# Kernel optimization log

Measured on AMD Instinct MI355X. Metric: run time of the kernel, lower is better.

## Reference

```python
import jax, jax.numpy as jnp
import numpy as np
import math

B, N, IN_DIM, HID, OUT = 16, 1024, 3, 32, 4
RATIO = 0.2
K1 = math.ceil(RATIO * N)    # 205 nodes kept after pool 1
K2 = math.ceil(RATIO * K1)   # 41 nodes kept after pool 2
AVG_DEG = 16.0
BN_EPS = 1e-5


def setup_inputs() -> dict:
    key = jax.random.key(0)
    ks = jax.random.split(key, 16)
    x = jax.random.normal(ks[0], (B, N, IN_DIM), jnp.float32)
    # sparse random undirected adjacency (binary edge weights = 1), no self loops
    u = jax.random.uniform(ks[1], (B, N, N))
    A = (u < (AVG_DEG / N)).astype(jnp.float32)
    A = jnp.maximum(A, jnp.swapaxes(A, -1, -2))
    A = A * (1.0 - jnp.eye(N, dtype=jnp.float32))
    g = lambda i, shp: (jax.random.normal(ks[i], shp, jnp.float32) * 0.1)
    params = dict(
        Wd0=g(2, (IN_DIM, HID)), bd0=jnp.zeros((HID,), jnp.float32),
        Wd1=g(3, (HID, HID)),    bd1=jnp.zeros((HID,), jnp.float32),
        Wd2=g(4, (HID, HID)),    bd2=jnp.zeros((HID,), jnp.float32),
        Wu0=g(5, (HID, HID)),    bu0=jnp.zeros((HID,), jnp.float32),
        Wu1=g(6, (HID, HID)),    bu1=jnp.zeros((HID,), jnp.float32),
        p1=g(7, (HID,)), p2=g(8, (HID,)),
        gamma=jnp.ones((HID,), jnp.float32), beta=jnp.zeros((HID,), jnp.float32),
        W1=g(9, (HID, HID)),  b1=jnp.zeros((HID,), jnp.float32),
        W2=g(10, (HID, HID)), b2=jnp.zeros((HID,), jnp.float32),
        W3=g(11, (HID, OUT)), b3=jnp.zeros((OUT,), jnp.float32),
    )
    return {"x": x, "adj": A, **params}


def _gcn(A, x, W, b):
    # GCNConv(improved=True): A_hat = A + 2I, symmetric normalization
    n = A.shape[-1]
    A_hat = A + 2.0 * jnp.eye(n, dtype=A.dtype)
    deg = A_hat.sum(-1)                              # [B, n]
    dis = jnp.where(deg > 0, jax.lax.rsqrt(deg), 0.0)
    A_norm = dis[..., :, None] * A_hat * dis[..., None, :]
    return jnp.einsum('bij,bjf->bif', A_norm, x @ W) + b


def _augment(A):
    # GraphUNet.augment_adj: add self loops (w=1), square adjacency, drop diag
    n = A.shape[-1]
    eye = jnp.eye(n, dtype=A.dtype)
    Bm = A + eye
    A2 = jnp.einsum('bij,bjk->bik', Bm, Bm)
    return A2 * (1.0 - eye)


def _topk_pool(A, x, p, k):
    # TopKPooling: score = tanh(x.p / ||p||), keep top-k nodes per graph
    score = jnp.tanh((x @ p) / jnp.linalg.norm(p))   # [B, n]
    vals, perm = jax.lax.top_k(score, k)             # descending, matches PyG
    bidx = jnp.arange(x.shape[0])[:, None]
    x_p = x[bidx, perm] * vals[..., None]
    A_p = A[bidx[..., None], perm[:, :, None], perm[:, None, :]]
    return A_p, x_p, perm


def reference(x, adj, Wd0, bd0, Wd1, bd1, Wd2, bd2, Wu0, bu0, Wu1, bu1,
              p1, p2, gamma, beta, W1, b1, W2, b2, W3, b3):
    bidx = jnp.arange(x.shape[0])[:, None]
    # ---- GraphUNet down path ----
    h0 = jax.nn.relu(_gcn(adj, x, Wd0, bd0))
    A1, h, perm1 = _topk_pool(_augment(adj), h0, p1, K1)
    h1 = jax.nn.relu(_gcn(A1, h, Wd1, bd1))
    A2, h, perm2 = _topk_pool(_augment(A1), h1, p2, K2)
    h = jax.nn.relu(_gcn(A2, h, Wd2, bd2))
    # ---- up path (sum_res=True) ----
    up = jnp.zeros_like(h1).at[bidx, perm2].set(h)
    h = jax.nn.relu(_gcn(A1, h1 + up, Wu0, bu0))
    up = jnp.zeros_like(h0).at[bidx, perm1].set(h)
    h = _gcn(adj, h0 + up, Wu1, bu1)   # last up conv: no activation
    # ---- BatchNorm1d over all nodes (training-mode batch stats, biased var) ----
    mean = h.mean((0, 1))
    var = h.var((0, 1))
    hn = (h - mean) * jax.lax.rsqrt(var + BN_EPS) * gamma + beta
    # ---- outnetwork MLP (dropout = identity in eval), LeakyReLU slope 0.01 ----
    r = jax.nn.leaky_relu(hn @ W1 + b1)
    r = jax.nn.leaky_relu(r @ W2 + b2)
    r = r @ W3 + b3
    return r.at[..., 0].set(jax.nn.sigmoid(r[..., 0]))
```

## Files before the change

kernel.cpp:

```cpp
#include <hip/hip_runtime.h>
#include <cmath>

#define BB 16
#define NN 1024
#define KK1 205
#define KK2 42
#define CAP 96
#define CHUNKS1 52
#define NREP 64

__global__ void k_deg_csr(const float* __restrict__ adj, const float* __restrict__ x,
                          const float* __restrict__ W,
                          float* __restrict__ dis0, int* __restrict__ ncnt,
                          int* __restrict__ nbr, unsigned long long* __restrict__ mask,
                          float* __restrict__ dxw, float* __restrict__ pacc) {
  if (blockIdx.x == 0) {
    for (int q = threadIdx.x; q < NREP * 64; q += 256) pacc[q] = 0.f;
  }
  int row = blockIdx.x * 4 + (threadIdx.x >> 6);
  int lane = threadIdx.x & 63;
  const float* ar = adj + (size_t)row * NN;
  float v[16];
#pragma unroll
  for (int c = 0; c < 16; ++c) v[c] = ar[c * 64 + lane];
  int base = 0;
  int* nr = nbr + (size_t)row * CAP;
#pragma unroll
  for (int c = 0; c < 16; ++c) {
    unsigned long long m = __ballot(v[c] != 0.0f);
    if (lane == c) mask[(size_t)row * 16 + c] = m;
    if (v[c] != 0.0f) {
      int pos = base + __popcll(m & ((1ull << lane) - 1ull));
      if (pos < CAP) nr[pos] = c * 64 + lane;
    }
    base += __popcll(m);
  }
  float dis = rsqrtf((float)base + 2.0f);
  if (lane == 0) {
    ncnt[row] = base < CAP ? base : CAP;
    dis0[row] = dis;
  }
  if (lane < 32) {
    float x0 = x[row * 3], x1 = x[row * 3 + 1], x2 = x[row * 3 + 2];
    float s = x0 * W[lane] + x1 * W[32 + lane] + x2 * W[64 + lane];
    dxw[(size_t)row * 32 + lane] = s * dis;
  }
}

template<bool RELU, bool SCORE, bool BNSTATS>
__global__ __launch_bounds__(256) void k_spmm_lds(
    const float* __restrict__ dxw, const float* __restrict__ dis,
    const int* __restrict__ ncnt, const int* __restrict__ nbr,
    const float* __restrict__ bias, float* __restrict__ out,
    float* __restrict__ score, const float* __restrict__ p,
    float* __restrict__ pacc) {
  __shared__ float sdxw[NN * 32];
  __shared__ float bs[8][32], bq[8][32];
  int tid = threadIdx.x;
  int b = blockIdx.x >> 4, chunk = blockIdx.x & 15;
  {
    const float4* src = (const float4*)(dxw + ((size_t)b * NN) * 32);
    float4* dst = (float4*)sdxw;
    for (int q = tid; q < NN * 8; q += 256) dst[q] = src[q];
  }
  __syncthreads();
  int g = tid >> 5, f = tid & 31;
  float bia = bias[f];
  float pv = SCORE ? p[f] : 0.f;
  float S = 0.f, Q = 0.f;
#pragma unroll
  for (int it = 0; it < 8; ++it) {
    int li = chunk * 64 + g * 8 + it;
    int node = b * NN + li;
    int cnt = ncnt[node];
    const int* lst = nbr + (size_t)node * CAP;
    float a0 = 0.f, a1 = 0.f, a2 = 0.f, a3 = 0.f;
    int k = 0;
    for (; k + 4 <= cnt; k += 4) {
      int4 j4 = *(const int4*)(lst + k);
      a0 += sdxw[j4.x * 32 + f];
      a1 += sdxw[j4.y * 32 + f];
      a2 += sdxw[j4.z * 32 + f];
      a3 += sdxw[j4.w * 32 + f];
    }
    for (; k < cnt; ++k) a0 += sdxw[lst[k] * 32 + f];
    float acc = (a0 + a1) + (a2 + a3) + 2.0f * sdxw[li * 32 + f];
    float r = dis[node] * acc + bia;
    if (RELU) r = fmaxf(r, 0.f);
    out[(size_t)node * 32 + f] = r;
    if (SCORE) {
      float d = r * pv, pp = pv * pv;
#pragma unroll
      for (int o = 16; o; o >>= 1) { d += __shfl_xor(d, o, 32); pp += __shfl_xor(pp, o, 32); }
      if (f == 0) score[node] = tanhf(d / sqrtf(pp));
    }
    if (BNSTATS) { S += r; Q += r * r; }
  }
  if (BNSTATS) {
    bs[g][f] = S; bq[g][f] = Q;
    __syncthreads();
    if (tid < 32) {
      float SS = 0.f, QQ = 0.f;
#pragma unroll
      for (int q = 0; q < 8; ++q) { SS += bs[q][tid]; QQ += bq[q][tid]; }
      int rep = blockIdx.x & (NREP - 1);
      atomicAdd(&pacc[rep * 64 + tid], SS);
      atomicAdd(&pacc[rep * 64 + 32 + tid], QQ);
    }
  }
}

__global__ __launch_bounds__(256) void k_sortA1(
    const unsigned long long* __restrict__ mask, const float* __restrict__ score1,
    const float* __restrict__ h0, const float* __restrict__ Wd1,
    float* __restrict__ A1, float* __restrict__ dis1, float* __restrict__ t1,
    int* __restrict__ inv1) {
  __shared__ union {
    unsigned long long skey[1024];
    unsigned long long smT[16 * KK1];
  } sm;
  __shared__ int sp[KK1];
  __shared__ float sval[KK1];
  int blk = blockIdx.x;
  int b = blk / CHUNKS1, chunk = blk - b * CHUNKS1;
  int t = threadIdx.x;
  for (int idx = t; idx < 1024; idx += 256) {
    float v = score1[b * NN + idx];
    unsigned int u = __float_as_uint(v);
    if (u == 0x80000000u) u = 0u;
    unsigned int ordv = (u & 0x80000000u) ? ~u : (u | 0x80000000u);
    if (chunk == 0) inv1[b * NN + idx] = -1;
    sm.skey[idx] = ((unsigned long long)(~ordv) << 32) | (unsigned)idx;
  }
  __syncthreads();
  for (int k = 2; k <= 1024; k <<= 1)
    for (int j = k >> 1; j > 0; j >>= 1) {
      for (int idx = t; idx < 1024; idx += 256) {
        int ixj = idx ^ j;
        if (ixj > idx) {
          unsigned long long a = sm.skey[idx], c = sm.skey[ixj];
          bool up = ((idx & k) == 0);
          if (up == (a > c)) { sm.skey[idx] = c; sm.skey[ixj] = a; }
        }
      }
      __syncthreads();
    }
  if (t < KK1) {
    unsigned long long kk = sm.skey[t];
    unsigned int ord = ~(unsigned int)(kk >> 32);
    unsigned int u = (ord & 0x80000000u) ? (ord & 0x7FFFFFFFu) : ~ord;
    int src = (int)(kk & 0xFFFFFFFFull);
    sp[t] = src;
    sval[t] = __uint_as_float(u);
    if (chunk == 0) inv1[b * NN + src] = t;
  }
  __syncthreads();
  for (int q = t; q < KK1 * 16; q += 256) {
    int i = q >> 4, w = q & 15;
    sm.smT[w * KK1 + i] = mask[((size_t)(b * NN + sp[i])) * 16 + w];
  }
  __syncthreads();
  int wave = t >> 6, lane = t & 63;
  int i = chunk * 4 + wave;
  if (i < KK1) {
    unsigned long long r[16];
#pragma unroll
    for (int w = 0; w < 16; ++w) r[w] = sm.smT[w * KK1 + i];
    float rowsum = 0.f;
    for (int j = lane; j < KK1; j += 64) {
      int cnt = 0;
#pragma unroll
      for (int w = 0; w < 16; ++w) cnt += __popcll(r[w] & sm.smT[w * KK1 + j]);
      int pj = sp[j];
      float edge = (float)((r[pj >> 6] >> (pj & 63)) & 1ull);
      float v = (j == i) ? 0.f : ((float)cnt + 2.f * edge);
      A1[((size_t)(b * KK1) + i) * KK1 + j] = v;
      rowsum += v;
    }
#pragma unroll
    for (int o = 32; o; o >>= 1) rowsum += __shfl_xor(rowsum, o);
    float dis = rsqrtf(rowsum + 2.0f);
    if (lane == 0) dis1[b * KK1 + i] = dis;
    if (lane < 32) {
      const float* hr = h0 + (size_t)(b * NN + sp[i]) * 32;
      float s = 0.f;
#pragma unroll
      for (int k = 0; k < 32; ++k) s += hr[k] * Wd1[k * 32 + lane];
      t1[((size_t)(b * KK1) + i) * 32 + lane] = s * dis * sval[i];
    }
  }
}

template<bool RELU, bool SCORE>
__global__ __launch_bounds__(256) void k_dense_apply(
    const float* __restrict__ A, const float* __restrict__ tbuf,
    const float* __restrict__ dis, const float* __restrict__ bias,
    int M, float* __restrict__ out, float* __restrict__ score,
    const float* __restrict__ p) {
  int row = blockIdx.x;
  int b = row / M, i = row - b * M;
  int tid = threadIdx.x;
  int g = tid >> 5, f = tid & 31;
  const float* Ar = A + (size_t)row * M;
  const float* tb = tbuf + (size_t)b * M * 32;
  float acc = 0.f;
  for (int j = g; j < M; j += 8)
    acc += Ar[j] * tb[j * 32 + f];
  __shared__ float ls[8][32];
  ls[g][f] = acc;
  __syncthreads();
  if (tid < 32) {
    float s = 0.f;
#pragma unroll
    for (int q = 0; q < 8; ++q) s += ls[q][tid];
    s += 2.0f * tb[i * 32 + tid];
    float r = dis[row] * s + bias[tid];
    if (RELU) r = fmaxf(r, 0.f);
    out[(size_t)row * 32 + tid] = r;
    if (SCORE) {
      float pv = p[tid];
      float d = r * pv, pp = pv * pv;
#pragma unroll
      for (int o = 16; o; o >>= 1) { d += __shfl_xor(d, o, 32); pp += __shfl_xor(pp, o, 32); }
      if (tid == 0) score[row] = tanhf(d / sqrtf(pp));
    }
  }
}

__global__ __launch_bounds__(256) void k_buildA2s(
    const float* __restrict__ score2, const float* __restrict__ A1,
    const float* __restrict__ h1, const float* __restrict__ Wd2,
    float* __restrict__ A2, float* __restrict__ dis2, float* __restrict__ t2,
    int* __restrict__ inv2) {
  __shared__ unsigned long long skey[256];
  __shared__ int sp2[KK2];
  __shared__ float sv2[KK2];
  __shared__ float gsum[8];
  __shared__ float ds2s;
  int row = blockIdx.x;
  int b = row / KK2, i = row - b * KK2;
  int t = threadIdx.x;
  {
    unsigned int ordv;
    if (t < KK1) {
      float v = score2[b * KK1 + t];
      unsigned int u = __float_as_uint(v);
      if (u == 0x80000000u) u = 0u;
      ordv = (u & 0x80000000u) ? ~u : (u | 0x80000000u);
      if (i == 0) inv2[b * KK1 + t] = -1;
    } else ordv = 0u;
    skey[t] = ((unsigned long long)(~ordv) << 32) | (unsigned)t;
  }
  __syncthreads();
  for (int k = 2; k <= 256; k <<= 1)
    for (int j = k >> 1; j > 0; j >>= 1) {
      int ixj = t ^ j;
      if (ixj > t) {
        unsigned long long a = skey[t], c = skey[ixj];
        bool up = ((t & k) == 0);
        if (up == (a > c)) { skey[t] = c; skey[ixj] = a; }
      }
      __syncthreads();
    }
  if (t < KK2) {
    unsigned long long kk = skey[t];
    unsigned int ord = ~(unsigned int)(kk >> 32);
    unsigned int u = (ord & 0x80000000u) ? (ord & 0x7FFFFFFFu) : ~ord;
    int src = (int)(kk & 0xFFFFFFFFull);
    sp2[t] = src;
    sv2[t] = __uint_as_float(u);
    if (i == 0) inv2[b * KK1 + src] = t;
  }
  __syncthreads();
  int g = t >> 5, lane = t & 31;
  int pi = sp2[i];
  const float* Ri = A1 + ((size_t)(b * KK1 + pi)) * KK1;
  float part = 0.f;
  for (int j = g; j < KK2; j += 8) {
    const float* Rj = A1 + ((size_t)(b * KK1 + sp2[j])) * KK1;
    float s = 0.f;
    for (int k = lane; k < KK1; k += 32) s += Ri[k] * Rj[k];
#pragma unroll
    for (int o = 16; o; o >>= 1) s += __shfl_xor(s, o, 32);
    float v = (i == j) ? 0.f : (s + 2.0f * Ri[sp2[j]]);
    if (lane == 0) {
      A2[(size_t)row * KK2 + j] = v;
      part += v;
    }
  }
  if (lane == 0) gsum[g] = part;
  __syncthreads();
  if (t == 0) {
    float s = 0.f;
#pragma unroll
    for (int q = 0; q < 8; ++q) s += gsum[q];
    float d2 = rsqrtf(s + 2.0f);
    dis2[row] = d2;
    ds2s = d2;
  }
  __syncthreads();
  if (t < 32) {
    const float* hr = h1 + (size_t)(b * KK1 + pi) * 32;
    float s = 0.f;
#pragma unroll
    for (int k = 0; k < 32; ++k) s += hr[k] * Wd2[k * 32 + t];
    t2[(size_t)row * 32 + t] = s * ds2s * sv2[i];
  }
}

__global__ void k_xw32u(const float* __restrict__ h, const float* __restrict__ up,
                        const int* __restrict__ inv, const float* __restrict__ W,
                        const float* __restrict__ dis, int M, int K,
                        float* __restrict__ out) {
  int idx = blockIdx.x * 256 + threadIdx.x;
  int f = idx & 31; int node = idx >> 5;
  int b = node / M;
  int iv = inv[node];
  const float* xr = h + (size_t)node * 32;
  float s = 0.f;
  if (iv >= 0) {
    const float* ur = up + (size_t)(b * K + iv) * 32;
#pragma unroll
    for (int k = 0; k < 32; ++k) s += (xr[k] + ur[k]) * W[k * 32 + f];
  } else {
#pragma unroll
    for (int k = 0; k < 32; ++k) s += xr[k] * W[k * 32 + f];
  }
  out[idx] = s * dis[node];
}

__global__ __launch_bounds__(64) void k_mlp(
    const float* __restrict__ h, const float* __restrict__ pacc,
    const float* __restrict__ gamma, const float* __restrict__ beta,
    const float* __restrict__ W1, const float* __restrict__ b1,
    const float* __restrict__ W2, const float* __restrict__ b2,
    const float* __restrict__ W3, const float* __restrict__ b3,
    float* __restrict__ out) {
  __shared__ float sW1[1024], sW2[1024], sW3[128];
  __shared__ float sb1[32], sb2[32], sb3[4], sscale[32], sshift[32];
  __shared__ float red[64];
  int t = threadIdx.x;
  {
    const float4* W1v = (const float4*)W1; float4* d1 = (float4*)sW1;
#pragma unroll
    for (int i = 0; i < 4; ++i) d1[t + i * 64] = W1v[t + i * 64];
    const float4* W2v = (const float4*)W2; float4* d2 = (float4*)sW2;
#pragma unroll
    for (int i = 0; i < 4; ++i) d2[t + i * 64] = W2v[t + i * 64];
    if (t < 32) ((float4*)sW3)[t] = ((const float4*)W3)[t];
    if (t < 32) { sb1[t] = b1[t]; sb2[t] = b2[t]; }
    if (t < 4) sb3[t] = b3[t];
    float a0 = 0.f, a1 = 0.f, a2 = 0.f, a3 = 0.f;
#pragma unroll
    for (int rep = 0; rep < NREP; rep += 4) {
      a0 += pacc[(rep + 0) * 64 + t]; a1 += pacc[(rep + 1) * 64 + t];
      a2 += pacc[(rep + 2) * 64 + t]; a3 += pacc[(rep + 3) * 64 + t];
    }
    red[t] = (a0 + a1) + (a2 + a3);
  }
  __syncthreads();
  if (t < 32) {
    const float inv = 1.0f / (float)(BB * NN);
    float m = red[t] * inv;
    float v = red[32 + t] * inv - m * m;
    float sc = gamma[t] * rsqrtf(v + 1e-5f);
    sscale[t] = sc;
    sshift[t] = beta[t] - m * sc;
  }
  __syncthreads();
  int node = blockIdx.x * 64 + t;
  const float4* hr = (const float4*)(h + (size_t)node * 32);
  float hn[32];
#pragma unroll
  for (int i = 0; i < 8; ++i) {
    float4 x = hr[i];
    hn[i * 4 + 0] = x.x * sscale[i * 4 + 0] + sshift[i * 4 + 0];
    hn[i * 4 + 1] = x.y * sscale[i * 4 + 1] + sshift[i * 4 + 1];
    hn[i * 4 + 2] = x.z * sscale[i * 4 + 2] + sshift[i * 4 + 2];
    hn[i * 4 + 3] = x.w * sscale[i * 4 + 3] + sshift[i * 4 + 3];
  }
  float r1[32];
#pragma unroll
  for (int f = 0; f < 32; ++f) r1[f] = sb1[f];
#pragma unroll
  for (int k = 0; k < 32; ++k) {
    float a = hn[k];
#pragma unroll
    for (int f = 0; f < 32; ++f) r1[f] += a * sW1[k * 32 + f];
  }
#pragma unroll
  for (int f = 0; f < 32; ++f) r1[f] = r1[f] > 0.f ? r1[f] : 0.01f * r1[f];
  float r2[32];
#pragma unroll
  for (int f = 0; f < 32; ++f) r2[f] = sb2[f];
#pragma unroll
  for (int k = 0; k < 32; ++k) {
    float a = r1[k];
#pragma unroll
    for (int f = 0; f < 32; ++f) r2[f] += a * sW2[k * 32 + f];
  }
#pragma unroll
  for (int f = 0; f < 32; ++f) r2[f] = r2[f] > 0.f ? r2[f] : 0.01f * r2[f];
  float r3[4];
#pragma unroll
  for (int c = 0; c < 4; ++c) r3[c] = sb3[c];
#pragma unroll
  for (int k = 0; k < 32; ++k) {
    float a = r2[k];
#pragma unroll
    for (int c = 0; c < 4; ++c) r3[c] += a * sW3[k * 4 + c];
  }
  float4 o;
  o.x = 1.0f / (1.0f + expf(-r3[0]));
  o.y = r3[1]; o.z = r3[2]; o.w = r3[3];
  ((float4*)out)[node] = o;
}

extern "C" void kernel_launch(void* const* d_in, const int* in_sizes, int n_in,
                              void* d_out, int out_size, void* d_ws, size_t ws_size,
                              hipStream_t stream) {
  const float* x    = (const float*)d_in[0];
  const float* adj  = (const float*)d_in[1];
  const float* Wd0  = (const float*)d_in[2];
  const float* bd0  = (const float*)d_in[3];
  const float* Wd1  = (const float*)d_in[4];
  const float* bd1  = (const float*)d_in[5];
  const float* Wd2  = (const float*)d_in[6];
  const float* bd2  = (const float*)d_in[7];
  const float* Wu0  = (const float*)d_in[8];
  const float* bu0  = (const float*)d_in[9];
  const float* Wu1  = (const float*)d_in[10];
  const float* bu1  = (const float*)d_in[11];
  const float* p1   = (const float*)d_in[12];
  const float* p2   = (const float*)d_in[13];
  const float* gamma= (const float*)d_in[14];
  const float* beta = (const float*)d_in[15];
  const float* W1   = (const float*)d_in[16];
  const float* b1   = (const float*)d_in[17];
  const float* W2   = (const float*)d_in[18];
  const float* b2   = (const float*)d_in[19];
  const float* W3   = (const float*)d_in[20];
  const float* b3   = (const float*)d_in[21];
  float* out = (float*)d_out;

  char* w = (char*)d_ws;
  auto alloc = [&](size_t bytes) -> void* {
    void* p = (void*)w;
    w += (bytes + 255) & ~(size_t)255;
    return p;
  };
  float* dis0 = (float*)alloc(BB * NN * 4);
  int*   ncnt = (int*)alloc(BB * NN * 4);
  int*   nbr  = (int*)alloc((size_t)BB * NN * CAP * 4);
  unsigned long long* mask = (unsigned long long*)alloc((size_t)BB * NN * 16 * 8);
  float* dxw  = (float*)alloc((size_t)BB * NN * 32 * 4);
  float* h0   = (float*)alloc((size_t)BB * NN * 32 * 4);
  float* score1 = (float*)alloc(BB * NN * 4);
  int*   inv1 = (int*)alloc(BB * NN * 4);
  float* A1   = (float*)alloc((size_t)BB * KK1 * KK1 * 4);
  float* dis1 = (float*)alloc(BB * KK1 * 4);
  float* t1   = (float*)alloc((size_t)BB * KK1 * 32 * 4);
  float* h1   = (float*)alloc((size_t)BB * KK1 * 32 * 4);
  float* score2 = (float*)alloc(BB * KK1 * 4);
  int*   inv2 = (int*)alloc(BB * KK1 * 4);
  float* A2   = (float*)alloc((size_t)BB * KK2 * KK2 * 4);
  float* dis2 = (float*)alloc(BB * KK2 * 4);
  float* t2   = (float*)alloc((size_t)BB * KK2 * 32 * 4);
  float* h2   = (float*)alloc((size_t)BB * KK2 * 32 * 4);
  float* hu0  = (float*)alloc((size_t)BB * KK1 * 32 * 4);
  float* hfin = (float*)alloc((size_t)BB * NN * 32 * 4);
  float* pacc = (float*)alloc((size_t)NREP * 64 * 4);

  const int TOT_N32  = BB * NN * 32;
  const int TOT_K132 = BB * KK1 * 32;

  k_deg_csr<<<BB * NN / 4, 256, 0, stream>>>(adj, x, Wd0, dis0, ncnt, nbr, mask, dxw, pacc);
  k_spmm_lds<true, true, false><<<BB * 16, 256, 0, stream>>>(
      dxw, dis0, ncnt, nbr, bd0, h0, score1, p1, nullptr);
  k_sortA1<<<BB * CHUNKS1, 256, 0, stream>>>(mask, score1, h0, Wd1, A1, dis1, t1, inv1);
  k_dense_apply<true, true><<<BB * KK1, 256, 0, stream>>>(
      A1, t1, dis1, bd1, KK1, h1, score2, p2);
  k_buildA2s<<<BB * KK2, 256, 0, stream>>>(score2, A1, h1, Wd2, A2, dis2, t2, inv2);
  k_dense_apply<true, false><<<BB * KK2, 256, 0, stream>>>(
      A2, t2, dis2, bd2, KK2, h2, nullptr, nullptr);
  k_xw32u<<<TOT_K132 / 256, 256, 0, stream>>>(h1, h2, inv2, Wu0, dis1, KK1, KK2, t1);
  k_dense_apply<true, false><<<BB * KK1, 256, 0, stream>>>(
      A1, t1, dis1, bu0, KK1, hu0, nullptr, nullptr);
  k_xw32u<<<TOT_N32 / 256, 256, 0, stream>>>(h0, hu0, inv1, Wu1, dis0, NN, KK1, dxw);
  k_spmm_lds<false, false, true><<<BB * 16, 256, 0, stream>>>(
      dxw, dis0, ncnt, nbr, bu1, hfin, nullptr, nullptr, pacc);
  k_mlp<<<BB * NN / 64, 64, 0, stream>>>(hfin, pacc, gamma, beta,
                                         W1, b1, W2, b2, W3, b3, out);
}
```

Baseline: 343.1 us.

## Fuse final up-path transform into SpMM and use register/shuffle bitonic sorts

The separate k_xw32u launch for the last up-path layer is removed. k_spmm_fused now loads h0, hu0 and inv1 into LDS and computes (h0+up)·Wu1·dis in place before the sparse aggregation and batch-norm statistics. Each of the 16 chunk blocks per graph recomputes the full 1024-row transform, trading redundant arithmetic for one fewer launch and one fewer global round trip. The top-k bitonic sorts in k_sortA1 and k_buildA2s keep keys in registers and exchange them with wave shuffles, touching LDS only for strides of 64 or more, which cuts barrier count. LDS use in the fused kernel sits near the per-workgroup limit.

```diff
diff --git a/kernel.cpp b/kernel.cpp
--- a/kernel.cpp
+++ b/kernel.cpp
@@ -9,6 +9,31 @@
 #define CHUNKS1 52
 #define NREP 64
 
+__device__ __forceinline__ void cswap(unsigned long long& a, unsigned long long& b,
+                                      bool asc) {
+  unsigned long long lo = a < b ? a : b;
+  unsigned long long hi = a < b ? b : a;
+  a = asc ? lo : hi;
+  b = asc ? hi : lo;
+}
+__device__ __forceinline__ unsigned long long pickmm(unsigned long long a,
+                                                     unsigned long long p,
+                                                     bool keepMin) {
+  unsigned long long mn = a < p ? a : p;
+  unsigned long long mx = a < p ? p : a;
+  return keepMin ? mn : mx;
+}
+__device__ __forceinline__ unsigned int ordkey(float v) {
+  unsigned int u = __float_as_uint(v);
+  if (u == 0x80000000u) u = 0u;
+  return (u & 0x80000000u) ? ~u : (u | 0x80000000u);
+}
+__device__ __forceinline__ float orddec(unsigned long long kk) {
+  unsigned int ord = ~(unsigned int)(kk >> 32);
+  unsigned int u = (ord & 0x80000000u) ? (ord & 0x7FFFFFFFu) : ~ord;
+  return __uint_as_float(u);
+}
+
 __global__ void k_deg_csr(const float* __restrict__ adj, const float* __restrict__ x,
                           const float* __restrict__ W,
                           float* __restrict__ dis0, int* __restrict__ ncnt,
@@ -47,15 +72,12 @@
   }
 }
 
-template<bool RELU, bool SCORE, bool BNSTATS>
 __global__ __launch_bounds__(256) void k_spmm_lds(
     const float* __restrict__ dxw, const float* __restrict__ dis,
     const int* __restrict__ ncnt, const int* __restrict__ nbr,
     const float* __restrict__ bias, float* __restrict__ out,
-    float* __restrict__ score, const float* __restrict__ p,
-    float* __restrict__ pacc) {
+    float* __restrict__ score, const float* __restrict__ p) {
   __shared__ float sdxw[NN * 32];
-  __shared__ float bs[8][32], bq[8][32];
   int tid = threadIdx.x;
   int b = blockIdx.x >> 4, chunk = blockIdx.x & 15;
   {
@@ -66,8 +88,7 @@
   __syncthreads();
   int g = tid >> 5, f = tid & 31;
   float bia = bias[f];
-  float pv = SCORE ? p[f] : 0.f;
-  float S = 0.f, Q = 0.f;
+  float pv = p[f];
 #pragma unroll
   for (int it = 0; it < 8; ++it) {
     int li = chunk * 64 + g * 8 + it;
@@ -85,28 +106,87 @@
     }
     for (; k < cnt; ++k) a0 += sdxw[lst[k] * 32 + f];
     float acc = (a0 + a1) + (a2 + a3) + 2.0f * sdxw[li * 32 + f];
+    float r = fmaxf(dis[node] * acc + bia, 0.f);
+    out[(size_t)node * 32 + f] = r;
+    float d = r * pv, pp = pv * pv;
+#pragma unroll
+    for (int o = 16; o; o >>= 1) { d += __shfl_xor(d, o, 32); pp += __shfl_xor(pp, o, 32); }
+    if (f == 0) score[node] = tanhf(d / sqrtf(pp));
+  }
+}
+
+__global__ __launch_bounds__(256) void k_spmm_fused(
+    const float* __restrict__ h0, const float* __restrict__ hu0,
+    const int* __restrict__ inv1, const float* __restrict__ Wu1,
+    const float* __restrict__ dis, const int* __restrict__ ncnt,
+    const int* __restrict__ nbr, const float* __restrict__ bias,
+    float* __restrict__ out, float* __restrict__ pacc) {
+  __shared__ float sH[NN * 32];
+  __shared__ float sUp[KK1 * 32];
+  __shared__ int sInv[NN];
+  int tid = threadIdx.x;
+  int b = blockIdx.x >> 4, chunk = blockIdx.x & 15;
+  {
+    const float4* src = (const float4*)(h0 + ((size_t)b * NN) * 32);
+    float4* dst = (float4*)sH;
+    for (int q = tid; q < NN * 8; q += 256) dst[q] = src[q];
+    const float4* us = (const float4*)(hu0 + ((size_t)b * KK1) * 32);
+    float4* ud = (float4*)sUp;
+    for (int q = tid; q < KK1 * 8; q += 256) ud[q] = us[q];
+    const int4* is = (const int4*)(inv1 + b * NN);
+    ((int4*)sInv)[tid] = is[tid];
+  }
+  __syncthreads();
+  int g = tid >> 5, f = tid & 31;
+  for (int r = g; r < NN; r += 8) {
+    int iv = sInv[r];
+    float s = 0.f;
+    if (iv >= 0) {
+#pragma unroll
+      for (int k = 0; k < 32; ++k)
+        s += (sH[r * 32 + k] + sUp[iv * 32 + k]) * Wu1[k * 32 + f];
+    } else {
+#pragma unroll
+      for (int k = 0; k < 32; ++k) s += sH[r * 32 + k] * Wu1[k * 32 + f];
+    }
+    s *= dis[b * NN + r];
+    sH[r * 32 + f] = s;
+  }
+  __syncthreads();
+  float bia = bias[f];
+  float S = 0.f, Q = 0.f;
+#pragma unroll
+  for (int it = 0; it < 8; ++it) {
+    int li = chunk * 64 + g * 8 + it;
+    int node = b * NN + li;
+    int cnt = ncnt[node];
+    const int* lst = nbr + (size_t)node * CAP;
+    float a0 = 0.f, a1 = 0.f, a2 = 0.f, a3 = 0.f;
+    int k = 0;
+    for (; k + 4 <= cnt; k += 4) {
+      int4 j4 = *(const int4*)(lst + k);
+      a0 += sH[j4.x * 32 + f];
+      a1 += sH[j4.y * 32 + f];
+      a2 += sH[j4.z * 32 + f];
+      a3 += sH[j4.w * 32 + f];
+    }
+    for (; k < cnt; ++k) a0 += sH[lst[k] * 32 + f];
+    float acc = (a0 + a1) + (a2 + a3) + 2.0f * sH[li * 32 + f];
     float r = dis[node] * acc + bia;
-    if (RELU) r = fmaxf(r, 0.f);
     out[(size_t)node * 32 + f] = r;
-    if (SCORE) {
-      float d = r * pv, pp = pv * pv;
-#pragma unroll
-      for (int o = 16; o; o >>= 1) { d += __shfl_xor(d, o, 32); pp += __shfl_xor(pp, o, 32); }
-      if (f == 0) score[node] = tanhf(d / sqrtf(pp));
-    }
-    if (BNSTATS) { S += r; Q += r * r; }
-  }
-  if (BNSTATS) {
-    bs[g][f] = S; bq[g][f] = Q;
-    __syncthreads();
-    if (tid < 32) {
-      float SS = 0.f, QQ = 0.f;
-#pragma unroll
-      for (int q = 0; q < 8; ++q) { SS += bs[q][tid]; QQ += bq[q][tid]; }
-      int rep = blockIdx.x & (NREP - 1);
-      atomicAdd(&pacc[rep * 64 + tid], SS);
-      atomicAdd(&pacc[rep * 64 + 32 + tid], QQ);
-    }
+    S += r; Q += r * r;
+  }
+  float* bs = sUp;
+  float* bq = sUp + 256;
+  bs[g * 32 + f] = S; bq[g * 32 + f] = Q;
+  __syncthreads();
+  if (tid < 32) {
+    float SS = 0.f, QQ = 0.f;
+#pragma unroll
+    for (int q = 0; q < 8; ++q) { SS += bs[q * 32 + tid]; QQ += bq[q * 32 + tid]; }
+    int rep = blockIdx.x & (NREP - 1);
+    atomicAdd(&pacc[rep * 64 + tid], SS);
+    atomicAdd(&pacc[rep * 64 + 32 + tid], QQ);
   }
 }
 
@@ -124,35 +204,60 @@
   int blk = blockIdx.x;
   int b = blk / CHUNKS1, chunk = blk - b * CHUNKS1;
   int t = threadIdx.x;
-  for (int idx = t; idx < 1024; idx += 256) {
-    float v = score1[b * NN + idx];
-    unsigned int u = __float_as_uint(v);
-    if (u == 0x80000000u) u = 0u;
-    unsigned int ordv = (u & 0x80000000u) ? ~u : (u | 0x80000000u);
-    if (chunk == 0) inv1[b * NN + idx] = -1;
-    sm.skey[idx] = ((unsigned long long)(~ordv) << 32) | (unsigned)idx;
-  }
-  __syncthreads();
-  for (int k = 2; k <= 1024; k <<= 1)
-    for (int j = k >> 1; j > 0; j >>= 1) {
-      for (int idx = t; idx < 1024; idx += 256) {
-        int ixj = idx ^ j;
-        if (ixj > idx) {
-          unsigned long long a = sm.skey[idx], c = sm.skey[ixj];
-          bool up = ((idx & k) == 0);
-          if (up == (a > c)) { sm.skey[idx] = c; sm.skey[ixj] = a; }
-        }
+  unsigned long long k0, k1, k2, k3;
+  {
+    const float* sc = score1 + b * NN;
+    int i0 = 4 * t;
+    if (chunk == 0) {
+      inv1[b * NN + i0] = -1; inv1[b * NN + i0 + 1] = -1;
+      inv1[b * NN + i0 + 2] = -1; inv1[b * NN + i0 + 3] = -1;
+    }
+    k0 = ((unsigned long long)(~ordkey(sc[i0 + 0])) << 32) | (unsigned)(i0 + 0);
+    k1 = ((unsigned long long)(~ordkey(sc[i0 + 1])) << 32) | (unsigned)(i0 + 1);
+    k2 = ((unsigned long long)(~ordkey(sc[i0 + 2])) << 32) | (unsigned)(i0 + 2);
+    k3 = ((unsigned long long)(~ordkey(sc[i0 + 3])) << 32) | (unsigned)(i0 + 3);
+  }
+  cswap(k0, k1, true); cswap(k2, k3, false);
+  for (int K = 4; K <= 1024; K <<= 1) {
+    bool up = ((t & (K >> 2)) == 0);
+    for (int j = K >> 1; j >= 4; j >>= 1) {
+      int d = j >> 2;
+      bool keepMin = (((t & d) == 0) == up);
+      if (d < 64) {
+        unsigned long long p0 = __shfl_xor(k0, d, 64);
+        unsigned long long p1 = __shfl_xor(k1, d, 64);
+        unsigned long long p2 = __shfl_xor(k2, d, 64);
+        unsigned long long p3 = __shfl_xor(k3, d, 64);
+        k0 = pickmm(k0, p0, keepMin); k1 = pickmm(k1, p1, keepMin);
+        k2 = pickmm(k2, p2, keepMin); k3 = pickmm(k3, p3, keepMin);
+      } else {
+        __syncthreads();
+        sm.skey[4 * t + 0] = k0; sm.skey[4 * t + 1] = k1;
+        sm.skey[4 * t + 2] = k2; sm.skey[4 * t + 3] = k3;
+        __syncthreads();
+        unsigned long long p0 = sm.skey[(4 * t + 0) ^ j];
+        unsigned long long p1 = sm.skey[(4 * t + 1) ^ j];
+        unsigned long long p2 = sm.skey[(4 * t + 2) ^ j];
+        unsigned long long p3 = sm.skey[(4 * t + 3) ^ j];
+        k0 = pickmm(k0, p0, keepMin); k1 = pickmm(k1, p1, keepMin);
+        k2 = pickmm(k2, p2, keepMin); k3 = pickmm(k3, p3, keepMin);
       }
-      __syncthreads();
-    }
-  if (t < KK1) {
-    unsigned long long kk = sm.skey[t];
-    unsigned int ord = ~(unsigned int)(kk >> 32);
-    unsigned int u = (ord & 0x80000000u) ? (ord & 0x7FFFFFFFu) : ~ord;
-    int src = (int)(kk & 0xFFFFFFFFull);
-    sp[t] = src;
-    sval[t] = __uint_as_float(u);
-    if (chunk == 0) inv1[b * NN + src] = t;
+    }
+    cswap(k0, k2, up); cswap(k1, k3, up);
+    cswap(k0, k1, up); cswap(k2, k3, up);
+  }
+  {
+    unsigned long long kk[4] = {k0, k1, k2, k3};
+#pragma unroll
+    for (int s = 0; s < 4; ++s) {
+      int idx = 4 * t + s;
+      if (idx < KK1) {
+        int src = (int)(kk[s] & 0xFFFFFFFFull);
+        sp[idx] = src;
+        sval[idx] = orddec(kk[s]);
+        if (chunk == 0) inv1[b * NN + src] = idx;
+      }
+    }
   }
   __syncthreads();
   for (int q = t; q < KK1 * 16; q += 256) {
@@ -240,35 +345,35 @@
   int row = blockIdx.x;
   int b = row / KK2, i = row - b * KK2;
   int t = threadIdx.x;
+  unsigned long long key;
   {
     unsigned int ordv;
     if (t < KK1) {
-      float v = score2[b * KK1 + t];
-      unsigned int u = __float_as_uint(v);
-      if (u == 0x80000000u) u = 0u;
-      ordv = (u & 0x80000000u) ? ~u : (u | 0x80000000u);
+      ordv = ordkey(score2[b * KK1 + t]);
       if (i == 0) inv2[b * KK1 + t] = -1;
     } else ordv = 0u;
-    skey[t] = ((unsigned long long)(~ordv) << 32) | (unsigned)t;
-  }
-  __syncthreads();
-  for (int k = 2; k <= 256; k <<= 1)
-    for (int j = k >> 1; j > 0; j >>= 1) {
-      int ixj = t ^ j;
-      if (ixj > t) {
-        unsigned long long a = skey[t], c = skey[ixj];
-        bool up = ((t & k) == 0);
-        if (up == (a > c)) { skey[t] = c; skey[ixj] = a; }
+    key = ((unsigned long long)(~ordv) << 32) | (unsigned)t;
+  }
+  for (int K = 2; K <= 256; K <<= 1) {
+    bool up = ((t & K) == 0);
+    for (int j = K >> 1; j >= 1; j >>= 1) {
+      bool keepMin = (((t & j) == 0) == up);
+      unsigned long long pk;
+      if (j < 64) {
+        pk = __shfl_xor(key, j, 64);
+      } else {
+        __syncthreads();
+        skey[t] = key;
+        __syncthreads();
+        pk = skey[t ^ j];
       }
-      __syncthreads();
-    }
+      key = pickmm(key, pk, keepMin);
+    }
+  }
   if (t < KK2) {
-    unsigned long long kk = skey[t];
-    unsigned int ord = ~(unsigned int)(kk >> 32);
-    unsigned int u = (ord & 0x80000000u) ? (ord & 0x7FFFFFFFu) : ~ord;
-    int src = (int)(kk & 0xFFFFFFFFull);
+    int src = (int)(key & 0xFFFFFFFFull);
     sp2[t] = src;
-    sv2[t] = __uint_as_float(u);
+    sv2[t] = orddec(key);
     if (i == 0) inv2[b * KK1 + src] = t;
   }
   __syncthreads();
@@ -471,12 +576,10 @@
   float* hfin = (float*)alloc((size_t)BB * NN * 32 * 4);
   float* pacc = (float*)alloc((size_t)NREP * 64 * 4);
 
-  const int TOT_N32  = BB * NN * 32;
   const int TOT_K132 = BB * KK1 * 32;
 
   k_deg_csr<<<BB * NN / 4, 256, 0, stream>>>(adj, x, Wd0, dis0, ncnt, nbr, mask, dxw, pacc);
-  k_spmm_lds<true, true, false><<<BB * 16, 256, 0, stream>>>(
-      dxw, dis0, ncnt, nbr, bd0, h0, score1, p1, nullptr);
+  k_spmm_lds<<<BB * 16, 256, 0, stream>>>(dxw, dis0, ncnt, nbr, bd0, h0, score1, p1);
   k_sortA1<<<BB * CHUNKS1, 256, 0, stream>>>(mask, score1, h0, Wd1, A1, dis1, t1, inv1);
   k_dense_apply<true, true><<<BB * KK1, 256, 0, stream>>>(
       A1, t1, dis1, bd1, KK1, h1, score2, p2);
@@ -486,9 +589,8 @@
   k_xw32u<<<TOT_K132 / 256, 256, 0, stream>>>(h1, h2, inv2, Wu0, dis1, KK1, KK2, t1);
   k_dense_apply<true, false><<<BB * KK1, 256, 0, stream>>>(
       A1, t1, dis1, bu0, KK1, hu0, nullptr, nullptr);
-  k_xw32u<<<TOT_N32 / 256, 256, 0, stream>>>(h0, hu0, inv1, Wu1, dis0, NN, KK1, dxw);
-  k_spmm_lds<false, false, true><<<BB * 16, 256, 0, stream>>>(
-      dxw, dis0, ncnt, nbr, bu1, hfin, nullptr, nullptr, pacc);
+  k_spmm_fused<<<BB * 16, 256, 0, stream>>>(h0, hu0, inv1, Wu1, dis0, ncnt, nbr,
+                                            bu1, hfin, pacc);
   k_mlp<<<BB * NN / 64, 64, 0, stream>>>(hfin, pacc, gamma, beta,
                                          W1, b1, W2, b2, W3, b3, out);
 }
```

After: 382.1 us. 11.4% more time.
